# Performance work log

Measured on AMD Instinct MI355X. Metric: run time of the kernel, lower is better.

The kernel has to match this reference:

```python
import jax, jax.numpy as jnp
from jax import lax
import numpy as np


def hac_round(X, W):
    """Avg-linkage HAC build+cut rounding of fractional SDP matrix X (D,D).
    Returns the 0/1 symmetric round_matrix with 1-diagonal."""
    D = X.shape[0]
    dt = X.dtype
    MAXD = jnp.max(jnp.abs(X)) * 1000.0  # _MAX_DIST sentinel
    max_sim = jnp.max(X)                 # max_similarity passed by forward()
    tril_mask = jnp.tril(jnp.ones((D, D), dtype=bool))
    # use_similarities=True branch: Y = MAXD*tril + (max_sim - X).triu(1)
    Y = jnp.where(tril_mask, MAXD, max_sim - X)
    values = jnp.min(Y, axis=1)
    indices = jnp.argmin(Y, axis=1)
    parents = jnp.arange(2 * D - 1)
    p2i = jnp.arange(2 * D - 1)   # parent_to_idx
    i2p = jnp.arange(D)           # idx_to_parent
    cs = jnp.ones(2 * D - 1, dtype=dt)
    energy = jnp.zeros(2 * D - 1, dtype=dt)
    clustering = jnp.zeros((2 * D - 1, D), dtype=dt)
    clustering = clustering.at[jnp.arange(D), jnp.arange(D)].set(jnp.arange(1, D + 1, dtype=dt))
    R = jnp.eye(D, dtype=dt)

    def body(i, st):
        Y, values, indices, parents, p2i, i2p, cs, energy, clustering, R = st
        max_node = D + i
        m1 = jnp.argmin(values)
        m2 = indices[m1]
        p1 = i2p[p2i[i2p[m1]]]
        p2 = i2p[p2i[i2p[m2]]]
        parents = parents.at[p1].set(max_node).at[p2].set(max_node)
        i2p = i2p.at[m1].set(max_node)
        p2i = p2i.at[max_node].set(m1)
        max_mask = Y == MAXD
        cs1, cs2 = cs[p1], cs[p2]
        ncs = cs1 + cs2
        cs = cs.at[max_node].set(ncs)
        # weighted average-linkage merged distances
        newv = (jnp.minimum(Y[m1, :], Y[:, m1]) * cs1 + jnp.minimum(Y[:, m2], Y[m2, :]) * cs2) / ncs
        Y = Y.at[:, m1].set(newv).at[m1, :].set(newv)
        Y = jnp.where(max_mask, MAXD, Y)
        Y = Y.at[:, m2].set(MAXD).at[m2, :].set(MAXD)
        values = values.at[m2].set(MAXD)
        vmask = values == MAXD
        values = jnp.where(vmask, MAXD, jnp.min(Y, axis=1))
        indices = jnp.argmin(Y, axis=1)
        # cut decision for the new internal node
        crow = clustering[p1] + clustering[p2]
        leaf = crow > 0                      # membership of new cluster
        lf = leaf.astype(dt)
        merge_e = lf @ (W @ lf)              # sum of W over leaf x leaf pairs
        e_sum = energy[p1] + energy[p2]
        take = merge_e >= e_sum
        energy = energy.at[max_node].set(jnp.where(take, merge_e, e_sum))
        crow = jnp.where(take & leaf, (max_node).astype(dt), crow)
        clustering = clustering.at[max_node].set(crow)
        R = jnp.where(take & (leaf[:, None] & leaf[None, :]), jnp.asarray(1.0, dt), R)
        return (Y, values, indices, parents, p2i, i2p, cs, energy, clustering, R)

    st = (Y, values, indices, parents, p2i, i2p, cs, energy, clustering, R)
    st = lax.fori_loop(0, D - 1, body, st)
    return st[-1]


def setup_inputs() -> dict:
    key = jax.random.key(0)
    k1, k2 = jax.random.split(key)
    D = 1024
    A = jax.random.uniform(k1, (D, D), dtype=jnp.float32)
    X = 0.5 * (A + A.T)                      # symmetric fractional decisions
    X = X.at[jnp.arange(D), jnp.arange(D)].set(1.0)  # 1-diagonal
    W = jnp.triu(jax.random.normal(k2, (D, D), dtype=jnp.float32), 1)  # triu(1) weights
    return {"X": X, "W": W}


def reference(X, W):
    # straight-through estimator: hard rounded solution, identity gradient w.r.t. X
    R = hac_round(X, W)
    return X + lax.stop_gradient(R - X)
```

## Files before the change

kernel.cpp:

```cpp
#include <hip/hip_runtime.h>
#include <stdint.h>

#define D 1024

typedef unsigned long long u64;
typedef unsigned int u32;

__device__ __forceinline__ u32 enc_f(float f) {
    u32 b = __float_as_uint(f);
    return (b & 0x80000000u) ? ~b : (b | 0x80000000u);
}
__device__ __forceinline__ float dec_f(u32 u) {
    u32 b = (u & 0x80000000u) ? (u ^ 0x80000000u) : ~u;
    return __uint_as_float(b);
}

__global__ void k_maxred(const float* __restrict__ X, u32* scal) {
    float mx = -INFINITY, ma = 0.f;
    int stride = gridDim.x * blockDim.x;
    for (int i = blockIdx.x * blockDim.x + threadIdx.x; i < D * D; i += stride) {
        float v = X[i];
        mx = fmaxf(mx, v);
        ma = fmaxf(ma, fabsf(v));
    }
    for (int o = 32; o; o >>= 1) {
        mx = fmaxf(mx, __shfl_xor(mx, o));
        ma = fmaxf(ma, __shfl_xor(ma, o));
    }
    if ((threadIdx.x & 63) == 0) {
        atomicMax(&scal[0], enc_f(mx));
        atomicMax(&scal[1], enc_f(ma));
    }
}

__global__ void k_init(const float* __restrict__ X, const float* __restrict__ W,
                       float2* __restrict__ dc, const u32* __restrict__ scal) {
    int idx = blockIdx.x * blockDim.x + threadIdx.x;
    if (idx >= D * D) return;
    float max_sim = dec_f(scal[0]);
    float MAXD = __fmul_rn(dec_f(scal[1]), 1000.0f);
    int i = idx >> 10, j = idx & (D - 1);
    float x = X[idx];
    float di = (i == j) ? MAXD : __fsub_rn(max_sim, x);
    float cx = (i == j) ? 0.0f : (W[idx] + W[j * D + i]);
    dc[idx] = make_float2(di, cx);
}

__global__ void k_rowmin(const float2* __restrict__ dc, float* __restrict__ values_g,
                         int* __restrict__ indices_g, const u32* __restrict__ scal) {
    int r = blockIdx.x;
    int lane = threadIdx.x;
    float MAXD = __fmul_rn(dec_f(scal[1]), 1000.0f);
    u64 best = ((u64)__float_as_uint(MAXD) << 32);
    const float4* row4 = (const float4*)(dc + (size_t)r * D);
    for (int c = lane; c < D / 2; c += 64) {
        float4 q = row4[c];
        int j0 = c << 1;
        if (j0 > r) {
            u64 k = ((u64)__float_as_uint(q.x) << 32) | (u32)j0;
            if (k < best) best = k;
        }
        if (j0 + 1 > r) {
            u64 k = ((u64)__float_as_uint(q.z) << 32) | (u32)(j0 + 1);
            if (k < best) best = k;
        }
    }
    for (int o = 32; o; o >>= 1) {
        u64 k2 = __shfl_xor(best, o);
        if (k2 < best) best = k2;
    }
    if (lane == 0) {
        values_g[r] = __uint_as_float((u32)(best >> 32));
        indices_g[r] = (int)(best & 0xffffffffu);
    }
}

__global__ void __launch_bounds__(1024) k_hac(
        float2* __restrict__ dc,
        const float* __restrict__ values_g, const int* __restrict__ indices_g,
        int* __restrict__ labels_g, const u32* __restrict__ scal) {
    __shared__ __align__(16) float values_l[D];
    __shared__ float values_stage[D];
    __shared__ int indices_l[D];
    __shared__ __align__(16) float newv_l[D];
    __shared__ float cs_l[D];
    __shared__ unsigned char dead_l[D];
    __shared__ unsigned char marked_l[D];
    __shared__ int slot_l[D];
    __shared__ int label_l[D];
    __shared__ double within_l[D];
    __shared__ double energy_l[D];
    __shared__ int rlist[2][D];
    __shared__ int nrec[2];
    __shared__ u64 s_best[2];
    __shared__ float s_cross12;
    __shared__ int s_takeP, s_m1P, s_labP;

    const int t = threadIdx.x;
    const int lane = t & 63, wid = t >> 6;
    const float MAXD = __fmul_rn(dec_f(scal[1]), 1000.0f);
    const u32 MAXDb = __float_as_uint(MAXD);

    values_l[t] = values_g[t];
    indices_l[t] = indices_g[t];
    cs_l[t] = 1.0f;
    dead_l[t] = 0;
    marked_l[t] = 0;
    slot_l[t] = t;
    label_l[t] = t;
    within_l[t] = 0.0;
    energy_l[t] = 0.0;
    if (t == 0) {
        s_takeP = 0; s_m1P = -1; s_labP = 0;
        nrec[0] = 0; nrec[1] = 0;
        s_best[0] = ~0ull; s_best[1] = ~0ull;
    }
    __syncthreads();
    {
        u64 key = ((u64)__float_as_uint(values_l[t]) << 32) | ((u32)t << 10) |
                  (u32)indices_l[t];
        for (int o = 32; o; o >>= 1) {
            u64 k2 = __shfl_xor(key, o);
            if (k2 < key) key = k2;
        }
        if (lane == 0) atomicMin(&s_best[0], key);
    }
    __syncthreads();

    for (int it = 0; it < D - 1; ++it) {
        const int cb = it & 1, pb = cb ^ 1;

        const u64 bk = s_best[cb];
        const int m1 = (int)((bk >> 10) & 1023);
        const int m2 = (int)(bk & 1023);
        const float cs1 = cs_l[m1], cs2 = cs_l[m2];
        const float ncs = __fadd_rn(cs1, cs2);
        const int pm1 = s_m1P;
        const int takeP = s_takeP, labP = s_labP;
        if (t == 0) s_best[pb] = ~0ull;

        if (marked_l[t]) { values_l[t] = values_stage[t]; marked_l[t] = 0; }
        if (t == m2) {
            dead_l[m2] = 1;
            values_l[m2] = MAXD;
            indices_l[m2] = 0;
        }
        const bool alive = !dead_l[t];

        float2 v1 = make_float2(0.f, 0.f), v2 = make_float2(0.f, 0.f);
        if (alive || t == m2) {
            v1 = dc[(size_t)m1 * D + t];
            v2 = dc[(size_t)m2 * D + t];
        }
        float d1 = v1.x, c1 = v1.y, d2 = v2.x, c2 = v2.y;

        {
            int sl = slot_l[t];
            if (takeP && sl == pm1) label_l[t] = labP;
            if (sl == m2) slot_l[t] = m1;
        }

        float nv = MAXD, ncx = 0.0f;
        bool do_st = false;
        if (t == m2) s_cross12 = c1;
        if (alive && t != m1) {
            nv = __fdiv_rn(__fadd_rn(__fmul_rn(d1, cs1), __fmul_rn(d2, cs2)), ncs);
            ncx = c1 + c2;
            dc[(size_t)m1 * D + t] = make_float2(nv, ncx);
            do_st = true;
        }
        newv_l[t] = nv;

        {
            float v = values_l[t];
            if (t == m1) {
                values_l[t] = MAXD;
                marked_l[t] = 1;
            } else if (alive && v < MAXD) {
                int idx = indices_l[t];
                if (idx == m2) {
                    rlist[cb][atomicAdd(&nrec[cb], 1)] = t;
                    values_l[t] = MAXD;
                    marked_l[t] = 1;
                } else if (idx == m1) {
                    if (nv <= v) values_l[t] = nv;
                    else {
                        rlist[cb][atomicAdd(&nrec[cb], 1)] = t;
                        values_l[t] = MAXD;
                        marked_l[t] = 1;
                    }
                } else if (t < m1) {
                    if (nv < v) { values_l[t] = nv; indices_l[t] = m1; }
                    else if (nv == v && m1 < idx) indices_l[t] = m1;
                }
            }
        }
        __syncthreads();

        if (t == m1) cs_l[m1] = ncs;
        const int n = nrec[cb];
        if (t == 0) nrec[pb] = 0;

        if (wid == 0) {
            if (do_st) dc[(size_t)t * D + m1] = make_float2(nv, ncx);
            if (lane == 0) {
                double merge_e = within_l[m1] + within_l[m2] + (double)s_cross12;
                double e_sum = energy_l[m1] + energy_l[m2];
                int take = (merge_e >= e_sum) ? 1 : 0;
                within_l[m1] = merge_e;
                energy_l[m1] = take ? merge_e : e_sum;
                s_takeP = take;
                s_m1P = m1;
                s_labP = D + it;
            }
            const float4* v4 = (const float4*)values_l;
            u64 bb = ~0ull;
#pragma unroll
            for (int c = 0; c < 4; ++c) {
                int fi = lane + 64 * c;
                float4 q = v4[fi];
                int b = fi << 2;
                u64 k;
                k = ((u64)__float_as_uint(q.x) << 32) | (u32)(b + 0); if (k < bb) bb = k;
                k = ((u64)__float_as_uint(q.y) << 32) | (u32)(b + 1); if (k < bb) bb = k;
                k = ((u64)__float_as_uint(q.z) << 32) | (u32)(b + 2); if (k < bb) bb = k;
                k = ((u64)__float_as_uint(q.w) << 32) | (u32)(b + 3); if (k < bb) bb = k;
            }
            for (int o = 32; o; o >>= 1) {
                u64 k2 = __shfl_xor(bb, o);
                if (k2 < bb) bb = k2;
            }
            if (lane == 0) {
                int r = (int)(bb & 1023);
                int idx = indices_l[r];
                atomicMin(&s_best[pb],
                          (bb & 0xffffffff00000000ull) | ((u32)r << 10) | (u32)idx);
            }
        } else if (wid == 1) {
            if (do_st) dc[(size_t)t * D + m1] = make_float2(nv, ncx);
            u64 bb = ((u64)MAXDb << 32);
            const float4* nv4 = (const float4*)newv_l;
            for (int c = lane; c < D / 4; c += 64) {
                float4 q = nv4[c];
                int j0 = c << 2;
#pragma unroll
                for (int e = 0; e < 4; ++e) {
                    int j = j0 + e;
                    float dv = (e == 0) ? q.x : (e == 1) ? q.y : (e == 2) ? q.z : q.w;
                    if (j > m1) {
                        u64 k = ((u64)__float_as_uint(dv) << 32) | (u32)j;
                        if (k < bb) bb = k;
                    }
                }
            }
            for (int o = 32; o; o >>= 1) {
                u64 k2 = __shfl_xor(bb, o);
                if (k2 < bb) bb = k2;
            }
            if (lane == 0) {
                values_stage[m1] = __uint_as_float((u32)(bb >> 32));
                indices_l[m1] = (int)(bb & 0xffffffffu);
                atomicMin(&s_best[pb],
                          (bb & 0xffffffff00000000ull) | ((u32)m1 << 10) | (bb & 1023));
            }
        } else {
            bool pend_st = do_st;
            for (int q = wid - 2; q < n; q += 14) {
                const int r = rlist[cb][q];
                const float subst = newv_l[r];
                const float4* row4 = (const float4*)(dc + (size_t)r * D);
                float4 a0 = row4[lane];
                float4 a1 = row4[lane + 64];
                float4 a2 = row4[lane + 128];
                float4 a3 = row4[lane + 192];
                float4 a4 = row4[lane + 256];
                float4 a5 = row4[lane + 320];
                float4 a6 = row4[lane + 384];
                float4 a7 = row4[lane + 448];
                if (pend_st) {
                    dc[(size_t)t * D + m1] = make_float2(nv, ncx);
                    pend_st = false;
                }
                u64 bb = ((u64)MAXDb << 32);
#define ACC2(af, koff)                                                          \
                {                                                               \
                    int j0 = (lane + (koff)) << 1;                              \
                    float dv0 = (j0 == m1) ? subst : (af).x;                    \
                    if (j0 > r && !dead_l[j0]) {                                \
                        u64 k = ((u64)__float_as_uint(dv0) << 32) | (u32)j0;    \
                        if (k < bb) bb = k;                                     \
                    }                                                           \
                    int j1 = j0 + 1;                                            \
                    float dv1 = (j1 == m1) ? subst : (af).z;                    \
                    if (j1 > r && !dead_l[j1]) {                                \
                        u64 k = ((u64)__float_as_uint(dv1) << 32) | (u32)j1;    \
                        if (k < bb) bb = k;                                     \
                    }                                                           \
                }
                ACC2(a0, 0)
                ACC2(a1, 64)
                ACC2(a2, 128)
                ACC2(a3, 192)
                ACC2(a4, 256)
                ACC2(a5, 320)
                ACC2(a6, 384)
                ACC2(a7, 448)
#undef ACC2
                for (int o = 32; o; o >>= 1) {
                    u64 k2 = __shfl_xor(bb, o);
                    if (k2 < bb) bb = k2;
                }
                if (lane == 0) {
                    values_stage[r] = __uint_as_float((u32)(bb >> 32));
                    indices_l[r] = (int)(bb & 0xffffffffu);
                    atomicMin(&s_best[pb],
                              (bb & 0xffffffff00000000ull) | ((u32)r << 10) | (bb & 1023));
                }
            }
            if (pend_st) dc[(size_t)t * D + m1] = make_float2(nv, ncx);
        }
        __syncthreads();
    }

    {
        int lab = label_l[t];
        if (s_takeP && slot_l[t] == s_m1P) lab = s_labP;
        labels_g[t] = lab;
    }
}

__global__ void k_out(const int* __restrict__ labels, float* __restrict__ out) {
    int idx = blockIdx.x * blockDim.x + threadIdx.x;
    if (idx >= D * D) return;
    int i = idx >> 10, j = idx & (D - 1);
    out[idx] = (i == j || labels[i] == labels[j]) ? 1.0f : 0.0f;
}

extern "C" void kernel_launch(void* const* d_in, const int* in_sizes, int n_in,
                              void* d_out, int out_size, void* d_ws, size_t ws_size,
                              hipStream_t stream) {
    const float* X = (const float*)d_in[0];
    const float* W = (const float*)d_in[1];

    char* ws = (char*)d_ws;
    const size_t MAT_BYTES = (size_t)D * D * sizeof(float);
    float2* dc = (float2*)ws;
    float* values_g = (float*)(ws + 2 * MAT_BYTES);
    int* indices_g = (int*)(ws + 2 * MAT_BYTES + 4096);
    int* labels_g = (int*)(ws + 2 * MAT_BYTES + 8192);
    u32* scal = (u32*)(ws + 2 * MAT_BYTES + 12288);

    hipMemsetAsync(scal, 0, 2 * sizeof(u32), stream);
    k_maxred<<<256, 256, 0, stream>>>(X, scal);
    k_init<<<(D * D) / 256, 256, 0, stream>>>(X, W, dc, scal);
    k_rowmin<<<D, 64, 0, stream>>>(dc, values_g, indices_g, scal);
    k_hac<<<1, 1024, 0, stream>>>(dc, values_g, indices_g, labels_g, scal);
    k_out<<<(D * D) / 256, 256, 0, stream>>>(labels_g, (float*)d_out);
}
```

Measured before the change: 3.181 ms.

## Forward previous merged row via LDS and use LDS-only barrier in HAC loop

```diff
diff --git a/kernel.cpp b/kernel.cpp
--- a/kernel.cpp
+++ b/kernel.cpp
@@ -13,6 +13,14 @@
 __device__ __forceinline__ float dec_f(u32 u) {
     u32 b = (u & 0x80000000u) ? (u ^ 0x80000000u) : ~u;
     return __uint_as_float(b);
+}
+
+__device__ __forceinline__ void barrier_lds_only() {
+    __builtin_amdgcn_sched_barrier(0);
+    asm volatile("s_waitcnt lgkmcnt(0)" ::: "memory");
+    __builtin_amdgcn_s_barrier();
+    asm volatile("" ::: "memory");
+    __builtin_amdgcn_sched_barrier(0);
 }
 
 __global__ void k_maxred(const float* __restrict__ X, u32* scal) {
@@ -82,7 +90,8 @@
     __shared__ __align__(16) float values_l[D];
     __shared__ float values_stage[D];
     __shared__ int indices_l[D];
-    __shared__ __align__(16) float newv_l[D];
+    __shared__ __align__(16) float newv_h[2][D];
+    __shared__ __align__(16) float crossv_h[2][D];
     __shared__ float cs_l[D];
     __shared__ unsigned char dead_l[D];
     __shared__ unsigned char marked_l[D];
@@ -147,12 +156,18 @@
         }
         const bool alive = !dead_l[t];
 
+        const bool h1 = (m1 == pm1), h2 = (m2 == pm1);
+
         float2 v1 = make_float2(0.f, 0.f), v2 = make_float2(0.f, 0.f);
         if (alive || t == m2) {
-            v1 = dc[(size_t)m1 * D + t];
-            v2 = dc[(size_t)m2 * D + t];
-        }
-        float d1 = v1.x, c1 = v1.y, d2 = v2.x, c2 = v2.y;
+            if (!h1) v1 = dc[(size_t)m1 * D + t];
+            if (!h2) v2 = dc[(size_t)m2 * D + t];
+        }
+        float d1, c1, d2, c2;
+        if (h1) { d1 = newv_h[pb][t]; c1 = crossv_h[pb][t]; }
+        else    { d1 = v1.x;          c1 = v1.y; }
+        if (h2) { d2 = newv_h[pb][t]; c2 = crossv_h[pb][t]; }
+        else    { d2 = v2.x;          c2 = v2.y; }
 
         {
             int sl = slot_l[t];
@@ -169,7 +184,8 @@
             dc[(size_t)m1 * D + t] = make_float2(nv, ncx);
             do_st = true;
         }
-        newv_l[t] = nv;
+        newv_h[cb][t] = nv;
+        crossv_h[cb][t] = ncx;
 
         {
             float v = values_l[t];
@@ -195,7 +211,7 @@
                 }
             }
         }
-        __syncthreads();
+        barrier_lds_only();
 
         if (t == m1) cs_l[m1] = ncs;
         const int n = nrec[cb];
@@ -239,7 +255,7 @@
         } else if (wid == 1) {
             if (do_st) dc[(size_t)t * D + m1] = make_float2(nv, ncx);
             u64 bb = ((u64)MAXDb << 32);
-            const float4* nv4 = (const float4*)newv_l;
+            const float4* nv4 = (const float4*)newv_h[cb];
             for (int c = lane; c < D / 4; c += 64) {
                 float4 q = nv4[c];
                 int j0 = c << 2;
@@ -267,7 +283,7 @@
             bool pend_st = do_st;
             for (int q = wid - 2; q < n; q += 14) {
                 const int r = rlist[cb][q];
-                const float subst = newv_l[r];
+                const float subst = newv_h[cb][r];
                 const float4* row4 = (const float4*)(dc + (size_t)r * D);
                 float4 a0 = row4[lane];
                 float4 a1 = row4[lane + 64];
```

Result: no change. 3.203 ms (+0.7%).
